# Optimization experiments

Hardware: AMD Instinct MI355X
Metric: run time of the kernel (lower is better)

## Reference

```python
import jax, jax.numpy as jnp
import numpy as np

B, D, T, H, E = 4, 1024, 2048, 16, 64  # batch, dim, seq_len, n_heads, hidden_dim (H*E == D)


def setup_inputs() -> dict:
    key = jax.random.key(0)
    ks = jax.random.split(key, 6)
    x = jax.random.normal(ks[0], (B, D, T), dtype=jnp.float32)            # (b, e, t) layout
    Wp = jax.random.normal(ks[1], (H, E, D), dtype=jnp.float32) / np.sqrt(D)  # per-head proj weights
    bp = jax.random.normal(ks[2], (H, E), dtype=jnp.float32) * 0.01
    tw = jax.random.normal(ks[3], (H, T), dtype=jnp.float32) / np.sqrt(T)  # per-head Toeplitz kernel, tw[h,0]=diagonal
    Wo = jax.random.normal(ks[4], (D, D), dtype=jnp.float32) / np.sqrt(D)
    bo = jax.random.normal(ks[5], (D,), dtype=jnp.float32) * 0.01
    return {"x": x, "Wp": Wp, "bp": bp, "tw": tw, "Wo": Wo, "bo": bo}


def reference(x, Wp, bp, tw, Wo, bo):
    # x: (b, dim, t) -> (b, t, dim)
    xt = jnp.transpose(x, (0, 2, 1))
    # per-head projections: (b, h, e, t)
    proj = jnp.einsum('btd,hed->bhet', xt, Wp) + bp[None, :, :, None]
    # build per-head causal lower-triangular Toeplitz matrices: Tm[h, t, s] = tw[h, t-s] if s <= t else 0
    idx = jnp.arange(T)[:, None] - jnp.arange(T)[None, :]  # (t, s)
    Tm = jnp.where(idx >= 0, tw[:, jnp.clip(idx, 0)], 0.0)  # (h, t, s)
    # causal Toeplitz mixing along time per head
    mixed = jnp.einsum('hts,bhes->bhet', Tm, proj)          # (b, h, e, t)
    # concat heads on feature dim: (b, t, h*e) == (b, t, dim)
    cat = jnp.transpose(mixed, (0, 3, 1, 2)).reshape(B, T, H * E)
    out = cat @ Wo.T + bo                                   # out_proj: Linear(dim, dim)
    return jnp.transpose(out, (0, 2, 1))                    # back to (b, e, t)
```

## Files before the change

### kernel.cpp

```cpp
#include <hip/hip_runtime.h>
#include <cstdint>

#define NB 4
#define ND 1024
#define NT 2048
#define NH 16
#define NE 64
#define GLEN 2240
#define CAP 2312

typedef __bf16 bf16x8 __attribute__((ext_vector_type(8)));
typedef float f32x4 __attribute__((ext_vector_type(4)));
typedef unsigned short us8 __attribute__((ext_vector_type(8)));
typedef unsigned short us4 __attribute__((ext_vector_type(4)));

__device__ __forceinline__ unsigned short f2bf(float f) {
  unsigned u = __builtin_bit_cast(unsigned, f);
  return (unsigned short)((u + 0x7fffu + ((u >> 16) & 1u)) >> 16);
}

__device__ __forceinline__ void gload16(const void* g, void* l) {
  __builtin_amdgcn_global_load_lds(
      (const __attribute__((address_space(1))) void*)(uintptr_t)g,
      (__attribute__((address_space(3))) void*)(uintptr_t)l, 16, 0, 0);
}

__global__ void prep_kernel(const float* __restrict__ Wp, const float* __restrict__ Wo,
                            const float* __restrict__ tw,
                            unsigned short* __restrict__ WpB, unsigned short* __restrict__ WoB,
                            unsigned short* __restrict__ Gr8) {
  int idx = blockIdx.x * 256 + threadIdx.x;
  int stride = gridDim.x * 256;
  const int n4 = ND * ND / 4;
  for (int i = idx; i < n4; i += stride) {
    float4 v = ((const float4*)Wp)[i];
    us4 o = {f2bf(v.x), f2bf(v.y), f2bf(v.z), f2bf(v.w)};
    ((us4*)WpB)[i] = o;
  }
  for (int i = idx; i < n4; i += stride) {
    float4 v = ((const float4*)Wo)[i];
    us4 o = {f2bf(v.x), f2bf(v.y), f2bf(v.z), f2bf(v.w)};
    ((us4*)WoB)[i] = o;
  }
  for (int i = idx; i < NH * 8 * GLEN; i += stride) {
    int h = i / (8 * GLEN);
    int rem = i - h * 8 * GLEN;
    int r = rem / GLEN;
    int c = rem - r * GLEN;
    int src = c + r;
    Gr8[i] = (src <= NT - 1) ? f2bf(tw[h * NT + (NT - 1) - src]) : (unsigned short)0;
  }
}

__global__ __launch_bounds__(256) void transpose_cast(const float* __restrict__ x,
                                                      unsigned short* __restrict__ xT) {
  __shared__ float tile[64][65];
  const int c = threadIdx.x & 15, r = threadIdx.x >> 4;
  const int t0 = blockIdx.x * 64, d0 = blockIdx.y * 64, b = blockIdx.z;
  const float* xb = x + (long)b * ND * NT;
#pragma unroll
  for (int k = 0; k < 4; ++k) {
    float4 v = *(const float4*)&xb[(long)(d0 + r + 16 * k) * NT + t0 + 4 * c];
    tile[r + 16 * k][4 * c + 0] = v.x;
    tile[r + 16 * k][4 * c + 1] = v.y;
    tile[r + 16 * k][4 * c + 2] = v.z;
    tile[r + 16 * k][4 * c + 3] = v.w;
  }
  __syncthreads();
  unsigned short* xTb = xT + (long)b * NT * ND;
#pragma unroll
  for (int k = 0; k < 4; ++k) {
    int t = r + 16 * k;
    us4 o = {f2bf(tile[4 * c + 0][t]), f2bf(tile[4 * c + 1][t]), f2bf(tile[4 * c + 2][t]),
             f2bf(tile[4 * c + 3][t])};
    *(us4*)&xTb[(long)(t0 + t) * ND + d0 + 4 * c] = o;
  }
}

template <bool OUT_BF16>
__global__ __launch_bounds__(256, 2) void gemm_bt(const unsigned short* __restrict__ A,
                                                  const unsigned short* __restrict__ Bt,
                                                  const float* __restrict__ bias,
                                                  void* __restrict__ Cb, long strideB,
                                                  long strideC) {
  const int N = 2048, K = 1024;
  __shared__ __align__(16) unsigned short As[2][2][128 * 32];
  __shared__ __align__(16) unsigned short Bs[2][2][128 * 32];
  const int tid = threadIdx.x;
  const int lane = tid & 63;
  const int wid = tid >> 6;
  const int wm = (wid & 1) * 64, wn = (wid >> 1) * 64;
  const int m0 = blockIdx.y * 128, n0 = blockIdx.x * 128;
  const unsigned short* Bb = Bt + (long)blockIdx.z * strideB;
  const int mlo = lane & 15, q = lane >> 4;

  f32x4 acc[4][4] = {};
  auto stage = [&](int buf, int k0) {
#pragma unroll
    for (int hh = 0; hh < 2; ++hh)
#pragma unroll
      for (int p = 0; p < 2; ++p) {
        int idx = p * 256 + tid;
        int row = idx >> 2, kc = (idx & 3) * 8;
        gload16(A + (long)(m0 + row) * K + k0 + hh * 32 + kc, &As[buf][hh][idx * 8]);
        gload16(Bb + (long)(n0 + row) * K + k0 + hh * 32 + kc, &Bs[buf][hh][idx * 8]);
      }
  };
  auto compute = [&](int buf) {
#pragma unroll
    for (int hh = 0; hh < 2; ++hh) {
      bf16x8 av[4], bv[4];
#pragma unroll
      for (int i = 0; i < 4; ++i) {
        av[i] =
            __builtin_bit_cast(bf16x8, *(const us8*)&As[buf][hh][(wm + i * 16 + mlo) * 32 + q * 8]);
        bv[i] =
            __builtin_bit_cast(bf16x8, *(const us8*)&Bs[buf][hh][(wn + i * 16 + mlo) * 32 + q * 8]);
      }
#pragma unroll
      for (int i = 0; i < 4; ++i)
#pragma unroll
        for (int j = 0; j < 4; ++j)
          acc[i][j] = __builtin_amdgcn_mfma_f32_16x16x32_bf16(av[i], bv[j], acc[i][j], 0, 0, 0);
    }
  };

  stage(0, 0);
#pragma unroll 1
  for (int k0 = 0; k0 < K; k0 += 128) {
    __syncthreads();
    stage(1, k0 + 64);
    compute(0);
    __syncthreads();
    if (k0 + 128 < K) stage(0, k0 + 128);
    compute(1);
  }
#pragma unroll
  for (int i = 0; i < 4; ++i)
#pragma unroll
    for (int j = 0; j < 4; ++j)
#pragma unroll
      for (int r = 0; r < 4; ++r) {
        int gr = m0 + wm + i * 16 + q * 4 + r;
        int gc = n0 + wn + j * 16 + mlo;
        float v = acc[i][j][r] + bias[gr];
        if (OUT_BF16)
          ((unsigned short*)Cb)[(long)blockIdx.z * strideC + (long)gr * N + gc] = f2bf(v);
        else
          ((float*)Cb)[(long)blockIdx.z * strideC + (long)gr * N + gc] = v;
      }
}

__global__ __launch_bounds__(256, 2) void toeplitz(const unsigned short* __restrict__ proj,
                                                   const unsigned short* __restrict__ Gr8,
                                                   unsigned short* __restrict__ mixedT) {
  __shared__ __align__(16) unsigned short Ls[8 * CAP];
  __shared__ __align__(16) unsigned short Bs[2][2][64 * 32];
  const int tid = threadIdx.x, lane = tid & 63, w = tid >> 6;
  const int j = blockIdx.x, h = blockIdx.y, bz = blockIdx.z;
  const int mlo = lane & 15, q = lane >> 4;
  const int wt = (w >> 1) * 64, we = (w & 1) * 32;
  const int t0L = (15 - j) * 128, t0S = j * 128;

  const int delta = (NT - 128) - t0L;
  const int MUSE = t0L + 256;
#pragma unroll 1
  for (int r = 0; r < 8; ++r) {
    int rr = (r + delta) & 7;
    int off8 = r + delta - rr;
    const unsigned short* src = Gr8 + (long)(h * 8 + rr) * GLEN + off8;
    unsigned short* dst = &Ls[r * CAP];
    for (int mc = tid; mc * 8 < MUSE; mc += 256) gload16(src + mc * 8, dst + mc * 8);
  }

  const int rA = (7 - mlo) & 7;
  const int eRow = tid >> 2, kCol = (tid & 3) * 8;
  const unsigned short* bsrc = proj + ((long)bz * ND + h * 64 + eRow) * NT + kCol;

#pragma unroll 1
  for (int p = 0; p < 2; ++p) {
    const int t0p = p ? t0S : t0L;
    const int kend = t0p + 128;
    const unsigned short* lA = &Ls[rA * CAP + (127 - wt - mlo - rA) + q * 8 + (t0L - t0p)];
    gload16(bsrc, &Bs[0][0][tid * 8]);
    gload16(bsrc + 32, &Bs[0][1][tid * 8]);
    __syncthreads();
    bf16x8 ap0 = __builtin_bit_cast(bf16x8, *(const us8*)(lA - 32));
    bf16x8 ap1 = __builtin_bit_cast(bf16x8, *(const us8*)(lA - 48));
    f32x4 acc[4][2] = {};

    auto sub = [&](int bf, int hh, int s) {
      bf16x8 a0 = __builtin_bit_cast(bf16x8, *(const us8*)(lA + s));
      bf16x8 a1 = __builtin_bit_cast(bf16x8, *(const us8*)(lA + s - 16));
      bf16x8 b0 = __builtin_bit_cast(bf16x8, *(const us8*)&Bs[bf][hh][(we + mlo) * 32 + q * 8]);
      bf16x8 b1 =
          __builtin_bit_cast(bf16x8, *(const us8*)&Bs[bf][hh][(we + 16 + mlo) * 32 + q * 8]);
      acc[0][0] = __builtin_amdgcn_mfma_f32_16x16x32_bf16(a0, b0, acc[0][0], 0, 0, 0);
      acc[0][1] = __builtin_amdgcn_mfma_f32_16x16x32_bf16(a0, b1, acc[0][1], 0, 0, 0);
      acc[1][0] = __builtin_amdgcn_mfma_f32_16x16x32_bf16(a1, b0, acc[1][0], 0, 0, 0);
      acc[1][1] = __builtin_amdgcn_mfma_f32_16x16x32_bf16(a1, b1, acc[1][1], 0, 0, 0);
      acc[2][0] = __builtin_amdgcn_mfma_f32_16x16x32_bf16(ap0, b0, acc[2][0], 0, 0, 0);
      acc[2][1] = __builtin_amdgcn_mfma_f32_16x16x32_bf16(ap0, b1, acc[2][1], 0, 0, 0);
      acc[3][0] = __builtin_amdgcn_mfma_f32_16x16x32_bf16(ap1, b0, acc[3][0], 0, 0, 0);
      acc[3][1] = __builtin_amdgcn_mfma_f32_16x16x32_bf16(ap1, b1, acc[3][1], 0, 0, 0);
      ap0 = a0;
      ap1 = a1;
    };

#pragma unroll 1
    for (int s0 = 0; s0 < kend; s0 += 128) {
      gload16(bsrc + s0 + 64, &Bs[1][0][tid * 8]);
      gload16(bsrc + s0 + 96, &Bs[1][1][tid * 8]);
      sub(0, 0, s0);
      sub(0, 1, s0 + 32);
      __syncthreads();
      if (s0 + 128 < kend) {
        gload16(bsrc + s0 + 128, &Bs[0][0][tid * 8]);
        gload16(bsrc + s0 + 160, &Bs[0][1][tid * 8]);
      }
      sub(1, 0, s0 + 64);
      sub(1, 1, s0 + 96);
      __syncthreads();
    }
#pragma unroll
    for (int i = 0; i < 4; ++i)
#pragma unroll
      for (int jj = 0; jj < 2; ++jj)
#pragma unroll
        for (int rr = 0; rr < 4; ++rr) {
          int t = t0p + wt + i * 16 + q * 4 + rr;
          int e = we + jj * 16 + mlo;
          mixedT[((long)bz * NT + t) * ND + h * 64 + e] = f2bf(acc[i][jj][rr]);
        }
  }
}

extern "C" void kernel_launch(void* const* d_in, const int* in_sizes, int n_in, void* d_out,
                              int out_size, void* d_ws, size_t ws_size, hipStream_t stream) {
  const float* x = (const float*)d_in[0];
  const float* Wp = (const float*)d_in[1];
  const float* bp = (const float*)d_in[2];
  const float* tw = (const float*)d_in[3];
  const float* Wo = (const float*)d_in[4];
  const float* bo = (const float*)d_in[5];
  float* out = (float*)d_out;

  char* ws = (char*)d_ws;
  unsigned short* xT = (unsigned short*)(ws);
  unsigned short* proj = (unsigned short*)(ws + (16ull << 20));
  unsigned short* WpB = (unsigned short*)(ws + (32ull << 20));
  unsigned short* WoB = (unsigned short*)(ws + (34ull << 20));
  unsigned short* Gr8 = (unsigned short*)(ws + (36ull << 20));

  prep_kernel<<<dim3(1024), 256, 0, stream>>>(Wp, Wo, tw, WpB, WoB, Gr8);
  transpose_cast<<<dim3(NT / 64, ND / 64, NB), 256, 0, stream>>>(x, xT);
  gemm_bt<true><<<dim3(16, 8, NB), 256, 0, stream>>>(WpB, xT, bp, proj, (long)NT * ND,
                                                     (long)ND * NT);
  toeplitz<<<dim3(8, NH, NB), 256, 0, stream>>>(proj, Gr8, xT);
  gemm_bt<false><<<dim3(16, 8, NB), 256, 0, stream>>>(WoB, xT, bo, out, (long)NT * ND,
                                                      (long)ND * NT);
}
```

Measured before the change: 167.7 us.

## Rework projection GEMMs into 512-thread, 128x256-tile, triple-buffered swizzled pipeline

The two bf16 GEMMs move to 512-thread blocks covering 128x256 output tiles, with 64-wide K steps held in a three-stage LDS ring. Loads for step t+2 are issued while step t computes, and manual vmcnt waits replace full __syncthreads. LDS rows use an XOR swizzle to avoid bank conflicts on the MFMA operand reads, and s_setprio raises priority around the MFMA bursts. The grid halves to 256 blocks per GEMM, which may reduce occupancy on the CU count, and the larger LDS footprint (about 144 KB) may limit residency to one block per CU.

```diff
diff --git a/kernel.cpp b/kernel.cpp
--- a/kernel.cpp
+++ b/kernel.cpp
@@ -78,63 +78,77 @@
 }
 
 template <bool OUT_BF16>
-__global__ __launch_bounds__(256, 2) void gemm_bt(const unsigned short* __restrict__ A,
+__global__ __launch_bounds__(512, 2) void gemm_bt(const unsigned short* __restrict__ A,
                                                   const unsigned short* __restrict__ Bt,
                                                   const float* __restrict__ bias,
                                                   void* __restrict__ Cb, long strideB,
                                                   long strideC) {
   const int N = 2048, K = 1024;
-  __shared__ __align__(16) unsigned short As[2][2][128 * 32];
-  __shared__ __align__(16) unsigned short Bs[2][2][128 * 32];
+  __shared__ __align__(16) unsigned short As[3][128 * 64];
+  __shared__ __align__(16) unsigned short Bs[3][256 * 64];
   const int tid = threadIdx.x;
   const int lane = tid & 63;
   const int wid = tid >> 6;
   const int wm = (wid & 1) * 64, wn = (wid >> 1) * 64;
-  const int m0 = blockIdx.y * 128, n0 = blockIdx.x * 128;
+  const int m0 = blockIdx.y * 128, n0 = blockIdx.x * 256;
   const unsigned short* Bb = Bt + (long)blockIdx.z * strideB;
-  const int mlo = lane & 15, q = lane >> 4;
+  const int mlo = lane & 15, q = lane >> 4, m7 = mlo & 7;
+
+  const int r0 = tid >> 3;
+  const int xblk = (tid & 7) ^ (r0 & 7);
+  const unsigned short* aSrc = A + (long)(m0 + r0) * K + xblk * 8;
+  const unsigned short* bSrc = Bb + (long)(n0 + r0) * K + xblk * 8;
+
+  auto stage0 = [&](int buf, int t) {
+    gload16(aSrc + t * 64, &As[buf][tid * 8]);
+    gload16(aSrc + 64 * (long)K + t * 64, &As[buf][(512 + tid) * 8]);
+    gload16(bSrc + t * 64, &Bs[buf][tid * 8]);
+  };
+  auto stage1 = [&](int buf, int t) {
+    gload16(bSrc + 64 * (long)K + t * 64, &Bs[buf][(512 + tid) * 8]);
+    gload16(bSrc + 128 * (long)K + t * 64, &Bs[buf][(1024 + tid) * 8]);
+    gload16(bSrc + 192 * (long)K + t * 64, &Bs[buf][(1536 + tid) * 8]);
+  };
 
   f32x4 acc[4][4] = {};
-  auto stage = [&](int buf, int k0) {
-#pragma unroll
-    for (int hh = 0; hh < 2; ++hh)
-#pragma unroll
-      for (int p = 0; p < 2; ++p) {
-        int idx = p * 256 + tid;
-        int row = idx >> 2, kc = (idx & 3) * 8;
-        gload16(A + (long)(m0 + row) * K + k0 + hh * 32 + kc, &As[buf][hh][idx * 8]);
-        gload16(Bb + (long)(n0 + row) * K + k0 + hh * 32 + kc, &Bs[buf][hh][idx * 8]);
-      }
-  };
-  auto compute = [&](int buf) {
-#pragma unroll
-    for (int hh = 0; hh < 2; ++hh) {
+  stage0(0, 0);
+  stage1(0, 0);
+  stage0(1, 1);
+  stage1(1, 1);
+
+#pragma unroll
+  for (int t = 0; t < 16; ++t) {
+    const int buf = t % 3;
+    if (t < 15)
+      asm volatile("s_waitcnt vmcnt(6) lgkmcnt(0)" ::: "memory");
+    else
+      asm volatile("s_waitcnt vmcnt(0) lgkmcnt(0)" ::: "memory");
+    __builtin_amdgcn_s_barrier();
+#pragma unroll
+    for (int ks = 0; ks < 2; ++ks) {
       bf16x8 av[4], bv[4];
+      const int xb8 = ((4 * ks + q) ^ m7) * 8;
 #pragma unroll
       for (int i = 0; i < 4; ++i) {
-        av[i] =
-            __builtin_bit_cast(bf16x8, *(const us8*)&As[buf][hh][(wm + i * 16 + mlo) * 32 + q * 8]);
-        bv[i] =
-            __builtin_bit_cast(bf16x8, *(const us8*)&Bs[buf][hh][(wn + i * 16 + mlo) * 32 + q * 8]);
-      }
+        av[i] = __builtin_bit_cast(bf16x8, *(const us8*)&As[buf][(wm + i * 16 + mlo) * 64 + xb8]);
+        bv[i] = __builtin_bit_cast(bf16x8, *(const us8*)&Bs[buf][(wn + i * 16 + mlo) * 64 + xb8]);
+      }
+      if (t + 2 < 16) {
+        if (ks == 0)
+          stage0((t + 2) % 3, t + 2);
+        else
+          stage1((t + 2) % 3, t + 2);
+      }
+      __builtin_amdgcn_s_setprio(1);
 #pragma unroll
       for (int i = 0; i < 4; ++i)
 #pragma unroll
         for (int j = 0; j < 4; ++j)
           acc[i][j] = __builtin_amdgcn_mfma_f32_16x16x32_bf16(av[i], bv[j], acc[i][j], 0, 0, 0);
+      __builtin_amdgcn_s_setprio(0);
     }
-  };
-
-  stage(0, 0);
-#pragma unroll 1
-  for (int k0 = 0; k0 < K; k0 += 128) {
-    __syncthreads();
-    stage(1, k0 + 64);
-    compute(0);
-    __syncthreads();
-    if (k0 + 128 < K) stage(0, k0 + 128);
-    compute(1);
-  }
+  }
+
 #pragma unroll
   for (int i = 0; i < 4; ++i)
 #pragma unroll
@@ -254,9 +268,9 @@
 
   prep_kernel<<<dim3(1024), 256, 0, stream>>>(Wp, Wo, tw, WpB, WoB, Gr8);
   transpose_cast<<<dim3(NT / 64, ND / 64, NB), 256, 0, stream>>>(x, xT);
-  gemm_bt<true><<<dim3(16, 8, NB), 256, 0, stream>>>(WpB, xT, bp, proj, (long)NT * ND,
+  gemm_bt<true><<<dim3(8, 8, NB), 512, 0, stream>>>(WpB, xT, bp, proj, (long)NT * ND,
+                                                    (long)ND * NT);
+  toeplitz<<<dim3(8, NH, NB), 256, 0, stream>>>(proj, Gr8, xT);
+  gemm_bt<false><<<dim3(8, 8, NB), 512, 0, stream>>>(WoB, xT, bo, out, (long)NT * ND,
                                                      (long)ND * NT);
-  toeplitz<<<dim3(8, NH, NB), 256, 0, stream>>>(proj, Gr8, xT);
-  gemm_bt<false><<<dim3(16, 8, NB), 256, 0, stream>>>(WoB, xT, bo, out, (long)NT * ND,
-                                                      (long)ND * NT);
-}
+}
```

After: 158.2 us. -5.7%, faster.
